# Kernel tuning notes

Measured on AMD Instinct MI355X. Metric: run time of the kernel, lower is better.

The kernel has to match this reference:

```python
import jax, jax.numpy as jnp
import numpy as np
import math

GRID_SIZE = 5
ORDER = 3
TAU = 0.1            # HuxleyRD tau (constructor default)
Q_SCALE = 64 / 2.0   # SaturatedQuantizer levels=64


def make_grid():
    h = 2.0 / GRID_SIZE
    # knots: arange(-order, grid_size+order+1)*h - 1  -> 12 values, shared by all in_features
    return jnp.arange(-ORDER, GRID_SIZE + ORDER + 1, dtype=jnp.float32) * h - 1.0


def b_splines(x, grid):
    # x: [b, in] -> bases: [b, in, GRID_SIZE+ORDER] via vectorized Cox-de Boor
    xg = x[..., None]
    g = grid  # [12], identical per feature so plain broadcasting suffices
    bases = ((xg >= g[:-1]) & (xg < g[1:])).astype(x.dtype)  # [b, in, 11]
    for p in range(1, ORDER + 1):
        t_i, t_ip = g[:-1 - p], g[p:-1]
        term1 = (xg - t_i) / (t_ip - t_i + 1e-8) * bases[..., :-1]
        t_i1, t_ip1 = g[1:-p], g[p + 1:]
        term2 = (t_ip1 - xg) / (t_ip1 - t_i1 + 1e-8) * bases[..., 1:]
        bases = term1 + term2
    return bases  # [b, in, 8]


def kan_layer(x, base_w, spline_w, grid):
    base = x @ base_w.T
    basis = b_splines(x, grid)
    # SaturatedQuantizer forward (round to levels); STE expressed via stop_gradient
    qw = spline_w + jax.lax.stop_gradient(jnp.round(spline_w * Q_SCALE) / Q_SCALE - spline_w)
    return base + jnp.einsum('bic,oic->bo', basis, qw)


def trig_unfolding(u, gcve_pressure, chirality, tau_decay):
    # u: [b, n]
    tr_c = jnp.sum(u * u, axis=-1)                                   # [b]
    uf_abs = jnp.abs(jnp.fft.rfft(u, axis=-1))                       # [b, n//2+1]
    det_pas = jnp.var(uf_abs, axis=-1, ddof=1) + 1e-6                # torch.var is unbiased
    denom = 2.0 * jnp.sqrt(det_pas) ** 3 + 1e-8
    cos_3phi = jnp.clip((3.0 * gcve_pressure - tr_c / tau_decay) / denom, -0.999, 0.999)
    phi = jnp.arccos(cos_3phi) / 3.0                                 # [b]
    lam_min = jnp.min(uf_abs, axis=-1)                               # [b]
    amp = 2.0 * jnp.sqrt(lam_min / 3.0 + 1e-8)                       # [b]
    ks = jnp.arange(3, dtype=u.dtype)                                # branch indices 0,1,2
    cos_terms = jnp.cos(phi[None, :] + 2.0 * jnp.pi * ks[:, None] / 3.0)   # [3, b]
    shifts = jnp.exp(-jnp.abs(chirality)[None, :] * ks[:, None])           # [3, b]
    coef = amp[None, :] * cos_terms * shifts                                # [3, b]
    branches = coef[:, :, None] * u[None, :, :]                             # [3, b, n]
    energies = jnp.linalg.norm(branches, axis=-1)                           # [3, b]
    best_k = jnp.argmax(energies, axis=0)                                   # [b]
    mask = (best_k[None, :] == jnp.arange(3)[:, None]).astype(u.dtype)      # [3, b]
    return jnp.sum(branches * mask[:, :, None], axis=0)


def huxley_rd(u, spectral_gate, kernel, a, gamma, tau_decay, soliton_velocity,
              gcve_pressure, chirality):
    N = u.shape[-1]
    # HarmonicWaveDecomposition: spectral sigmoid gate split
    uf = jnp.fft.rfft(u, axis=-1)
    gate = jax.nn.sigmoid(spectral_gate)
    u_erg = jnp.fft.irfft(uf * gate, n=N, axis=-1)
    u_ne = jnp.fft.irfft(uf * (1.0 - gate), n=N, axis=-1)
    # ergodic: cubic reaction + 3-tap diffusion conv (padding=1, cross-correlation)
    reaction = u_erg * (u_erg - a) * (1.0 - u_erg)
    up = jnp.pad(u_erg, ((0, 0), (1, 1)))
    diffusion = kernel[0] * up[:, :-2] + kernel[1] * up[:, 1:-1] + kernel[2] * up[:, 2:]
    u_erg_next = u_erg + TAU * (reaction + gamma * diffusion)
    # non-ergodic: spectral phase shift (soliton translation)
    nef = jnp.fft.rfft(u_ne, axis=-1)
    k_idx = jnp.arange(nef.shape[-1], dtype=jnp.float32)
    phase = jnp.exp(-1j * 2.0 * jnp.pi * k_idx * soliton_velocity / N)
    u_ne_shift = jnp.fft.irfft(nef * phase, n=N, axis=-1)
    u_ne_unf = trig_unfolding(u_ne_shift, gcve_pressure, chirality, tau_decay)
    s = u_erg_next + u_ne_unf
    return jax.nn.sigmoid(s) * s  # SiLU-style fusion


def setup_inputs() -> dict:
    key = jax.random.key(0)
    ks = jax.random.split(key, 12)
    B, NIN, W, NOUT = 4096, 512, 1024, 1024
    return {
        'c': jax.random.uniform(ks[0], (B, NIN), jnp.float32, -1.0, 1.0),
        'base_w0': jax.random.normal(ks[1], (W, NIN), jnp.float32) * (1.0 / np.sqrt(NIN)),
        'spline_w0': jax.random.normal(ks[2], (W, NIN, 8), jnp.float32) * 0.1,
        'base_w1': jax.random.normal(ks[3], (W, W), jnp.float32) * (1.0 / np.sqrt(W)),
        'spline_w1': jax.random.normal(ks[4], (W, W, 8), jnp.float32) * 0.1,
        'base_w2': jax.random.normal(ks[5], (NOUT, W), jnp.float32) * (1.0 / np.sqrt(W)),
        'spline_w2': jax.random.normal(ks[6], (NOUT, W, 8), jnp.float32) * 0.1,
        'spectral_gate': jnp.ones((NOUT // 2 + 1,), jnp.float32),
        'diffusion_kernel': jnp.asarray([0.1, -0.2, 0.1], jnp.float32),
        'a_param': jnp.asarray(0.1, jnp.float32),
        'gamma': jnp.asarray(1.0, jnp.float32),
        'tau_decay': jnp.asarray(0.1, jnp.float32),
        'soliton_velocity': jnp.asarray(0.25, jnp.float32),
        'gcve_pressure': jax.random.uniform(ks[7], (B,), jnp.float32),
        'chirality': jax.random.normal(ks[8], (B,), jnp.float32),
    }


def reference(c, base_w0, spline_w0, base_w1, spline_w1, base_w2, spline_w2,
              spectral_gate, diffusion_kernel, a_param, gamma, tau_decay,
              soliton_velocity, gcve_pressure, chirality):
    grid = make_grid()
    x = kan_layer(c, base_w0, spline_w0, grid)
    x = kan_layer(x, base_w1, spline_w1, grid)
    x = kan_layer(x, base_w2, spline_w2, grid)
    return huxley_rd(x, spectral_gate, diffusion_kernel, a_param, gamma,
                     tau_decay, soliton_velocity, gcve_pressure, chirality)
```

## Files before the change

### kernel.cpp

```cpp
#include <hip/hip_runtime.h>
#include <math.h>

typedef _Float16 f16;
typedef _Float16 f16x8 __attribute__((ext_vector_type(8)));
typedef float f32x4 __attribute__((ext_vector_type(4)));

__global__ __launch_bounds__(256) void expand_sum_a(
    const float* __restrict__ src, size_t plane, int Sin,
    f16* __restrict__ Aexp, int KIN, int shift)
{
    int idx = blockIdx.x * 256 + threadIdx.x;
    int i = idx & (KIN - 1);
    int b = idx >> shift;
    float x = 0.0f;
    for (int s = 0; s < Sin; ++s) x += src[(size_t)s * plane + idx];

    float xs = (x + 2.2f) * 2.5f;
    float fj = floorf(xs);
    int jj = (int)fj;
    float t = xs - fj;
    float t2 = t * t, t3 = t2 * t;
    float omt = 1.0f - t;
    float p0 = omt * omt * omt * (1.0f / 6.0f);
    float p1 = (3.0f * t3 - 6.0f * t2 + 4.0f) * (1.0f / 6.0f);
    float p2 = (-3.0f * t3 + 3.0f * t2 + 3.0f * t + 1.0f) * (1.0f / 6.0f);
    float p3 = t3 * (1.0f / 6.0f);

    union { f16 h[8]; uint4 v; } hi, lo;
    bool inr = (jj >= 0 && jj <= 10);
    #pragma unroll
    for (int cc = 0; cc < 8; ++cc) {
        int d = cc - (jj - 3);
        float v = 0.0f;
        if (inr) {
            if (d == 0) v = p0; else if (d == 1) v = p1;
            else if (d == 2) v = p2; else if (d == 3) v = p3;
        }
        f16 h = (f16)v;
        hi.h[cc] = h;
        lo.h[cc] = (f16)(v - (float)h);
    }
    size_t KEXP = (size_t)KIN * 19;
    f16* row = Aexp + (size_t)b * KEXP;
    *(uint4*)(row + (size_t)i * 8) = hi.v;
    *(uint4*)(row + (size_t)KIN * 8 + (size_t)i * 8) = lo.v;
    f16 xh = (f16)x;
    f16 xl = (f16)(x - (float)xh);
    int K16 = KIN * 16;
    row[K16 + i] = xh;
    row[K16 + KIN + i] = xh;
    row[K16 + 2 * KIN + i] = xl;
}

__global__ __launch_bounds__(256) void prep_b(
    const float* __restrict__ BW, const float* __restrict__ SW,
    f16* __restrict__ Bexp, int KIN, int shift)
{
    int idx = blockIdx.x * 256 + threadIdx.x;
    int i = idx & (KIN - 1);
    int o = idx >> shift;
    const float* sp = SW + ((size_t)o * KIN + i) * 8;
    union { f16 h[8]; uint4 v; } pk;
    #pragma unroll
    for (int cc = 0; cc < 8; ++cc)
        pk.h[cc] = (f16)(rintf(sp[cc] * 32.0f) * 0.03125f);
    size_t KEXP = (size_t)KIN * 19;
    f16* row = Bexp + (size_t)o * KEXP;
    *(uint4*)(row + (size_t)i * 8) = pk.v;
    *(uint4*)(row + (size_t)KIN * 8 + (size_t)i * 8) = pk.v;
    float w = BW[(size_t)o * KIN + i];
    f16 wh = (f16)w;
    f16 wl = (f16)(w - (float)wh);
    int K16 = KIN * 16;
    row[K16 + i] = wh;
    row[K16 + KIN + i] = wl;
    row[K16 + 2 * KIN + i] = wh;
}

__global__ __launch_bounds__(512, 2) void gemm_mfma(
    const f16* __restrict__ A, const f16* __restrict__ Bm,
    float* __restrict__ C, int Kfull, int Kc, size_t plane, int N)
{
    __shared__ __align__(16) f16 As[4][8192];
    __shared__ __align__(16) f16 Bs[4][8192];

    const int tid = threadIdx.x;
    const int wave = tid >> 6, lane = tid & 63;

    const int nwg = gridDim.x * gridDim.y * gridDim.z;
    const int b = blockIdx.x + gridDim.x * (blockIdx.y + gridDim.y * blockIdx.z);
    const int q = nwg >> 3;
    const int L = (b & 7) * q + (b >> 3);
    const int lx = L % gridDim.x;
    const int rest = L / gridDim.x;
    const int ly = rest % gridDim.y;
    const int lz = rest / gridDim.y;

    const int m0 = ly * 256, n0 = lx * 256;
    const int kb = lz * Kc;
    int kcl = Kfull - kb; if (kcl > Kc) kcl = Kc;
    const int NT = kcl >> 5;

    const int kc_src = (lane & 3) ^ ((lane >> 3) & 3);
    const f16* gb[4];
    int isA_[4], coff[4];
    #pragma unroll
    for (int j = 0; j < 4; ++j) {
        int cch = wave * 4 + j;
        int a = (cch < 16);
        int c8 = a ? cch : (cch - 16);
        int row0 = (a ? m0 : n0) + c8 * 16 + (lane >> 2);
        gb[j] = (a ? A : Bm) + (size_t)row0 * Kfull + kb + kc_src * 8;
        isA_[j] = a;
        coff[j] = c8 * 512;
    }

    f32x4 acc[8][4];
    #pragma unroll
    for (int i = 0; i < 8; ++i)
        #pragma unroll
        for (int j = 0; j < 4; ++j)
            acc[i][j] = (f32x4){0.f, 0.f, 0.f, 0.f};

    #pragma unroll
    for (int s = 0; s < 3; ++s) {
        if (s < NT) {
            int k0 = s << 5;
            #pragma unroll
            for (int j = 0; j < 4; ++j) {
                f16* dp = isA_[j] ? &As[s][coff[j]] : &Bs[s][coff[j]];
                __builtin_amdgcn_global_load_lds(
                    (const __attribute__((address_space(1))) unsigned int*)(gb[j] + k0),
                    (__attribute__((address_space(3))) unsigned int*)dp, 16, 0, 0);
            }
        }
    }
    if (NT >= 3)      asm volatile("s_waitcnt vmcnt(8)" ::: "memory");
    else if (NT == 2) asm volatile("s_waitcnt vmcnt(4)" ::: "memory");
    else              asm volatile("s_waitcnt vmcnt(0)" ::: "memory");
    __builtin_amdgcn_s_barrier();
    asm volatile("" ::: "memory");

    const int lr = lane & 15;
    const int ko = (((lane >> 4) ^ ((lr >> 1) & 3)) & 3) * 8;
    const int wm = (wave & 1) * 128, wn = (wave >> 1) * 64;

    for (int t = 0; t < NT; ++t) {
        const int st = t & 3;
        const int ns = (t + 3) & 3;
        const bool pf = (t + 3 < NT);
        const int kn = (t + 3) << 5;
        const int rem = NT - 1 - t;

        f16x8 af[4], bf[4], ag[4];
        #pragma unroll
        for (int i = 0; i < 4; ++i)
            af[i] = *(const f16x8*)&As[st][(wm + i * 16 + lr) * 32 + ko];
        #pragma unroll
        for (int j = 0; j < 4; ++j)
            bf[j] = *(const f16x8*)&Bs[st][(wn + j * 16 + lr) * 32 + ko];
        if (pf) {
            #pragma unroll
            for (int j = 0; j < 2; ++j) {
                f16* dp = isA_[j] ? &As[ns][coff[j]] : &Bs[ns][coff[j]];
                __builtin_amdgcn_global_load_lds(
                    (const __attribute__((address_space(1))) unsigned int*)(gb[j] + kn),
                    (__attribute__((address_space(3))) unsigned int*)dp, 16, 0, 0);
            }
        }
        #pragma unroll
        for (int i = 0; i < 4; ++i)
            ag[i] = *(const f16x8*)&As[st][(wm + 64 + i * 16 + lr) * 32 + ko];
        if (pf) {
            #pragma unroll
            for (int j = 2; j < 4; ++j) {
                f16* dp = isA_[j] ? &As[ns][coff[j]] : &Bs[ns][coff[j]];
                __builtin_amdgcn_global_load_lds(
                    (const __attribute__((address_space(1))) unsigned int*)(gb[j] + kn),
                    (__attribute__((address_space(3))) unsigned int*)dp, 16, 0, 0);
            }
        }

        asm volatile("s_waitcnt lgkmcnt(4)" ::: "memory");
        __builtin_amdgcn_sched_barrier(0);
        __builtin_amdgcn_s_setprio(1);
        #pragma unroll
        for (int i = 0; i < 4; ++i)
            #pragma unroll
            for (int j = 0; j < 4; ++j)
                acc[i][j] = __builtin_amdgcn_mfma_f32_16x16x32_f16(af[i], bf[j], acc[i][j], 0, 0, 0);
        __builtin_amdgcn_s_setprio(0);

        asm volatile("s_waitcnt lgkmcnt(0)" ::: "memory");
        __builtin_amdgcn_sched_barrier(0);
        __builtin_amdgcn_s_setprio(1);
        #pragma unroll
        for (int i = 0; i < 4; ++i)
            #pragma unroll
            for (int j = 0; j < 4; ++j)
                acc[4 + i][j] = __builtin_amdgcn_mfma_f32_16x16x32_f16(ag[i], bf[j], acc[4 + i][j], 0, 0, 0);
        __builtin_amdgcn_s_setprio(0);

        if (rem >= 3)      asm volatile("s_waitcnt vmcnt(8)" ::: "memory");
        else if (rem == 2) asm volatile("s_waitcnt vmcnt(4)" ::: "memory");
        else if (rem == 1) asm volatile("s_waitcnt vmcnt(0)" ::: "memory");
        if (rem >= 1) {
            __builtin_amdgcn_sched_barrier(0);
            __builtin_amdgcn_s_barrier();
            asm volatile("" ::: "memory");
        }
    }

    float* Cp = C + (size_t)lz * plane;
    #pragma unroll
    for (int i = 0; i < 8; ++i) {
        int row = m0 + wm + i * 16 + (lane >> 4) * 4;
        #pragma unroll
        for (int j = 0; j < 4; ++j) {
            int col = n0 + wn + j * 16 + lr;
            #pragma unroll
            for (int rr = 0; rr < 4; ++rr)
                Cp[(size_t)(row + rr) * N + col] = acc[i][j][rr];
        }
    }
}

__global__ __launch_bounds__(256) void kan_gemm(
    const float* __restrict__ X, const float* __restrict__ BW,
    const float* __restrict__ SW, float* __restrict__ Y, int KIN, int OUT)
{
    __shared__ __align__(16) float Asf[72][68];
    __shared__ __align__(16) float Bsf[72][68];
    const int tid = threadIdx.x;
    const int n0 = blockIdx.x * 64;
    const int m0 = blockIdx.y * 64;
    const int tx = tid & 15;
    const int ty = tid >> 4;
    float acc[4][4] = {};
    for (int k0 = 0; k0 < KIN; k0 += 8) {
        #pragma unroll
        for (int rep = 0; rep < 2; ++rep) {
            int idx = rep * 256 + tid;
            int r = idx >> 3, c = idx & 7;
            float x = X[(size_t)(m0 + r) * KIN + k0 + c];
            int bk = c * 9;
            Asf[bk][r] = x;
            #pragma unroll
            for (int z = 0; z < 8; ++z) Asf[bk + 1 + z][r] = 0.0f;
            float xs = (x + 2.2f) * 2.5f;
            float fj = floorf(xs);
            int j = (int)fj;
            if (j >= 0 && j <= 10) {
                float t = xs - fj;
                float t2 = t * t, t3 = t2 * t;
                float omt = 1.0f - t;
                float p0 = omt * omt * omt * (1.0f / 6.0f);
                float p1 = (3.0f * t3 - 6.0f * t2 + 4.0f) * (1.0f / 6.0f);
                float p2 = (-3.0f * t3 + 3.0f * t2 + 3.0f * t + 1.0f) * (1.0f / 6.0f);
                float p3 = t3 * (1.0f / 6.0f);
                if (j >= 3) Asf[bk + 1 + j - 3][r] = p0;
                if (j >= 2 && j <= 9) Asf[bk + 1 + j - 2][r] = p1;
                if (j >= 1 && j <= 8) Asf[bk + 1 + j - 1][r] = p2;
                if (j <= 7) Asf[bk + 1 + j][r] = p3;
            }
        }
        #pragma unroll
        for (int rep = 0; rep < 16; ++rep) {
            int idx = rep * 256 + tid;
            int ol = idx >> 6;
            int l = idx & 63;
            int i = l >> 3, cc = l & 7;
            float v = SW[((size_t)(n0 + ol) * KIN + k0 + i) * 8 + cc];
            Bsf[i * 9 + 1 + cc][ol] = rintf(v * 32.0f) * 0.03125f;
        }
        #pragma unroll
        for (int rep = 0; rep < 2; ++rep) {
            int idx = rep * 256 + tid;
            int ol = idx >> 3, cc = idx & 7;
            Bsf[cc * 9][ol] = BW[(size_t)(n0 + ol) * KIN + k0 + cc];
        }
        __syncthreads();
        #pragma unroll 8
        for (int kk = 0; kk < 72; ++kk) {
            float4 av = *(const float4*)&Asf[kk][ty * 4];
            float4 bv = *(const float4*)&Bsf[kk][tx * 4];
            acc[0][0] += av.x * bv.x; acc[0][1] += av.x * bv.y; acc[0][2] += av.x * bv.z; acc[0][3] += av.x * bv.w;
            acc[1][0] += av.y * bv.x; acc[1][1] += av.y * bv.y; acc[1][2] += av.y * bv.z; acc[1][3] += av.y * bv.w;
            acc[2][0] += av.z * bv.x; acc[2][1] += av.z * bv.y; acc[2][2] += av.z * bv.z; acc[2][3] += av.z * bv.w;
            acc[3][0] += av.w * bv.x; acc[3][1] += av.w * bv.y; acc[3][2] += av.w * bv.z; acc[3][3] += av.w * bv.w;
        }
        __syncthreads();
    }
    #pragma unroll
    for (int i = 0; i < 4; ++i) {
        float4 o = make_float4(acc[i][0], acc[i][1], acc[i][2], acc[i][3]);
        *(float4*)&Y[(size_t)(m0 + ty * 4 + i) * OUT + n0 + tx * 4] = o;
    }
}

__device__ __forceinline__ float block_reduce_sum(float v, float* red, int tid) {
    red[tid] = v; __syncthreads();
    #pragma unroll
    for (int s = 128; s > 0; s >>= 1) {
        if (tid < s) red[tid] += red[tid + s];
        __syncthreads();
    }
    float r = red[0]; __syncthreads();
    return r;
}
__device__ __forceinline__ float block_reduce_min(float v, float* red, int tid) {
    red[tid] = v; __syncthreads();
    #pragma unroll
    for (int s = 128; s > 0; s >>= 1) {
        if (tid < s) red[tid] = fminf(red[tid], red[tid + s]);
        __syncthreads();
    }
    float r = red[0]; __syncthreads();
    return r;
}

__device__ void fft1024(float2* X, const float2* tw, int tid, bool inverse) {
    if (!inverse) {
        for (int sh = 9; sh >= 0; --sh) {
            int h = 1 << sh;
            #pragma unroll
            for (int q = 0; q < 2; ++q) {
                int b = tid + q * 256;
                int g = b >> sh, j = b & (h - 1);
                int i0 = (g << (sh + 1)) + j, i1 = i0 + h;
                float2 u = X[i0], v = X[i1];
                float dx = u.x - v.x, dy = u.y - v.y;
                X[i0] = make_float2(u.x + v.x, u.y + v.y);
                float2 w = tw[j << (9 - sh)];
                X[i1] = make_float2(dx * w.x + dy * w.y, dy * w.x - dx * w.y);
            }
            __syncthreads();
        }
    } else {
        for (int sh = 0; sh <= 9; ++sh) {
            int h = 1 << sh;
            #pragma unroll
            for (int q = 0; q < 2; ++q) {
                int b = tid + q * 256;
                int g = b >> sh, j = b & (h - 1);
                int i0 = (g << (sh + 1)) + j, i1 = i0 + h;
                float2 u = X[i0], v = X[i1];
                float2 w = tw[j << (9 - sh)];
                float tx2 = v.x * w.x - v.y * w.y;
                float ty2 = v.x * w.y + v.y * w.x;
                X[i0] = make_float2(u.x + tx2, u.y + ty2);
                X[i1] = make_float2(u.x - tx2, u.y - ty2);
            }
            __syncthreads();
        }
    }
}

__global__ __launch_bounds__(256) void huxley_kernel(
    const float* __restrict__ Pin, size_t plane, int S,
    float* __restrict__ dst,
    const float* __restrict__ sg, const float* __restrict__ dk,
    const float* __restrict__ pa, const float* __restrict__ pgam,
    const float* __restrict__ ptau, const float* __restrict__ pvel,
    const float* __restrict__ gp, const float* __restrict__ chi)
{
    __shared__ float2 A[1024];
    __shared__ float2 Bb[1024];
    __shared__ float sErg[1024];
    __shared__ float sAbs[516];
    __shared__ float2 tw[512];
    __shared__ float red[256];
    __shared__ float sG[516];

    const int tid = threadIdx.x;
    const int row = blockIdx.x;
    const float* pin = Pin + (size_t)row * 1024;
    float* uo = dst + (size_t)row * 1024;

    for (int m = tid; m < 512; m += 256) {
        float s, c;
        sincosf(6.283185307179586f * (float)m * (1.0f / 1024.0f), &s, &c);
        tw[m] = make_float2(c, s);
    }
    for (int k = tid; k < 513; k += 256)
        sG[k] = 1.0f / (1.0f + expf(-sg[k]));
    for (int i = tid; i < 1024; i += 256) {
        float s = 0.0f;
        for (int ss = 0; ss < S; ++ss) s += pin[(size_t)ss * plane + i];
        A[i] = make_float2(s, 0.0f);
    }
    __syncthreads();

    fft1024(A, tw, tid, false);

    for (int p = tid; p < 1024; p += 256) {
        int k = (int)(__brev((unsigned)p) >> 22);
        int m = (k <= 512) ? k : 1024 - k;
        float g = sG[m] * (1.0f / 1024.0f);
        Bb[p] = make_float2(A[p].x * g, A[p].y * g);
    }
    __syncthreads();
    fft1024(Bb, tw, tid, true);
    for (int i = tid; i < 1024; i += 256) sErg[i] = Bb[i].x;
    __syncthreads();

    const float vv = pvel[0];
    for (int p = tid; p < 1024; p += 256) {
        int k = (int)(__brev((unsigned)p) >> 22);
        int m = (k <= 512) ? k : 1024 - k;
        float omg = 1.0f - sG[m];
        float nx = A[p].x * omg, ny = A[p].y * omg;
        float ang = (k <= 512)
            ? (-6.283185307179586f * vv * (float)k * (1.0f / 1024.0f))
            : (6.283185307179586f * vv * (float)(1024 - k) * (1.0f / 1024.0f));
        float sn, cs;
        sincosf(ang, &sn, &cs);
        float yx = nx * cs - ny * sn;
        float yy = nx * sn + ny * cs;
        if (k < 512)       sAbs[k]   = sqrtf(nx * nx + ny * ny);
        else if (k == 512) sAbs[512] = fabsf(yx);
        Bb[p] = make_float2(yx * (1.0f / 1024.0f), yy * (1.0f / 1024.0f));
    }
    __syncthreads();
    fft1024(Bb, tw, tid, true);

    float loc = 0.0f;
    for (int i = tid; i < 1024; i += 256) { float x = Bb[i].x; loc += x * x; }
    float trc = block_reduce_sum(loc, red, tid);

    loc = 0.0f;
    for (int k = tid; k < 513; k += 256) loc += sAbs[k];
    float mean = block_reduce_sum(loc, red, tid) * (1.0f / 513.0f);

    loc = 0.0f;
    for (int k = tid; k < 513; k += 256) { float d = sAbs[k] - mean; loc += d * d; }
    float varsum = block_reduce_sum(loc, red, tid);

    loc = 3.4e38f;
    for (int k = tid; k < 513; k += 256) loc = fminf(loc, sAbs[k]);
    float lmin = block_reduce_min(loc, red, tid);

    float det_pas = varsum * (1.0f / 512.0f) + 1e-6f;
    float sd = sqrtf(det_pas);
    float denom = 2.0f * sd * sd * sd + 1e-8f;
    float c3 = (3.0f * gp[row] - trc / ptau[0]) / denom;
    c3 = fminf(fmaxf(c3, -0.999f), 0.999f);
    float ph = acosf(c3) * (1.0f / 3.0f);
    float amp = 2.0f * sqrtf(lmin * (1.0f / 3.0f) + 1e-8f);
    float nu = sqrtf(trc);
    float achi = fabsf(chi[row]);
    float cbest = 0.0f, ebest = -1.0f;
    #pragma unroll
    for (int kb = 0; kb < 3; ++kb) {
        float ck = amp * cosf(ph + 2.0943951023931953f * (float)kb) * expf(-achi * (float)kb);
        float ek = fabsf(ck) * nu;
        if (ek > ebest) { ebest = ek; cbest = ck; }
    }

    const float a = pa[0], gm = pgam[0];
    const float k0 = dk[0], k1 = dk[1], k2 = dk[2];
    for (int i = tid; i < 1024; i += 256) {
        float e = sErg[i];
        float l = (i > 0) ? sErg[i - 1] : 0.0f;
        float r = (i < 1023) ? sErg[i + 1] : 0.0f;
        float reac = e * (e - a) * (1.0f - e);
        float diff = k0 * l + k1 * e + k2 * r;
        float un = e + 0.1f * (reac + gm * diff);
        float s = un + cbest * Bb[i].x;
        uo[i] = s / (1.0f + expf(-s));
    }
}


extern "C" void kernel_launch(void* const* d_in, const int* in_sizes, int n_in,
                              void* d_out, int out_size, void* d_ws, size_t ws_size,
                              hipStream_t stream) {
    const float* c    = (const float*)d_in[0];
    const float* bw0  = (const float*)d_in[1];
    const float* sw0  = (const float*)d_in[2];
    const float* bw1  = (const float*)d_in[3];
    const float* sw1  = (const float*)d_in[4];
    const float* bw2  = (const float*)d_in[5];
    const float* sw2  = (const float*)d_in[6];
    const float* sg   = (const float*)d_in[7];
    const float* dk   = (const float*)d_in[8];
    const float* pa   = (const float*)d_in[9];
    const float* pgam = (const float*)d_in[10];
    const float* ptau = (const float*)d_in[11];
    const float* pvel = (const float*)d_in[12];
    const float* gp   = (const float*)d_in[13];
    const float* chi  = (const float*)d_in[14];

    const int B = 4096, NIN = 512, W = 1024, NOUT = 1024;
    const int KE0 = 19 * NIN, KE1 = 19 * W;
    const size_t MN = (size_t)B * W;
    const size_t BE = (size_t)W * KE1 * 2;
    dim3 blk(256);
    dim3 gblk(512);

    struct Cand { int CH, S; };
    const Cand cands[] = {
        {4096, 4}, {4096, 3}, {2048, 4}, {2048, 3}, {1024, 4},
        {512, 4}, {256, 4}
    };
    int CH = 0, S = 1;
    for (const auto& cd : cands) {
        size_t need = BE + (size_t)cd.CH * KE1 * 2 + (size_t)cd.S * MN * 4;
        if (need <= ws_size) { CH = cd.CH; S = cd.S; break; }
    }

    if (CH > 0) {
        f16* Bexp = (f16*)d_ws;
        float* P  = (float*)((char*)d_ws + BE);
        f16* Aexp = (f16*)((char*)d_ws + BE + (size_t)S * MN * 4);

        const int Kc0 = ((KE0 / 32 + S - 1) / S) * 32;
        const int Kc1 = ((KE1 / 32 + S - 1) / S) * 32;

        prep_b<<<(W * NIN) / 256, blk, 0, stream>>>(bw0, sw0, Bexp, NIN, 9);
        for (int r0 = 0; r0 < B; r0 += CH) {
            expand_sum_a<<<(CH * NIN) / 256, blk, 0, stream>>>(
                c + (size_t)r0 * NIN, 0, 1, Aexp, NIN, 9);
            gemm_mfma<<<dim3(W / 256, CH / 256, S), gblk, 0, stream>>>(
                Aexp, Bexp, P + (size_t)r0 * W, KE0, Kc0, MN, W);
        }
        prep_b<<<(W * W) / 256, blk, 0, stream>>>(bw1, sw1, Bexp, W, 10);
        for (int r0 = 0; r0 < B; r0 += CH) {
            expand_sum_a<<<(CH * W) / 256, blk, 0, stream>>>(
                P + (size_t)r0 * W, MN, S, Aexp, W, 10);
            gemm_mfma<<<dim3(W / 256, CH / 256, S), gblk, 0, stream>>>(
                Aexp, Bexp, P + (size_t)r0 * W, KE1, Kc1, MN, W);
        }
        prep_b<<<(NOUT * W) / 256, blk, 0, stream>>>(bw2, sw2, Bexp, W, 10);
        for (int r0 = 0; r0 < B; r0 += CH) {
            expand_sum_a<<<(CH * W) / 256, blk, 0, stream>>>(
                P + (size_t)r0 * W, MN, S, Aexp, W, 10);
            gemm_mfma<<<dim3(NOUT / 256, CH / 256, S), gblk, 0, stream>>>(
                Aexp, Bexp, P + (size_t)r0 * W, KE1, Kc1, MN, NOUT);
        }
        huxley_kernel<<<B, blk, 0, stream>>>(P, MN, S, (float*)d_out,
                                             sg, dk, pa, pgam, ptau, pvel, gp, chi);
    } else {
        float* fx0 = (float*)d_ws;
        float* fx1 = fx0 + (size_t)B * W;
        dim3 g0(W / 64, B / 64);
        kan_gemm<<<g0, blk, 0, stream>>>(c,   bw0, sw0, fx0, NIN, W);
        kan_gemm<<<g0, blk, 0, stream>>>(fx0, bw1, sw1, fx1, W,   W);
        dim3 g2(NOUT / 64, B / 64);
        kan_gemm<<<g2, blk, 0, stream>>>(fx1, bw2, sw2, (float*)d_out, W, NOUT);
        huxley_kernel<<<B, blk, 0, stream>>>((float*)d_out, 0, 1, (float*)d_out,
                                             sg, dk, pa, pgam, ptau, pvel, gp, chi);
    }
}
```

Measured before the change: 678.2 us.

## Pack two real rows into one complex FFT in huxley kernel

The huxley kernel now handles two batch rows per block by placing them in the real and imaginary parts of a single complex 1024-point FFT. Each row's spectral magnitudes are recovered through conjugate-symmetric separation, and the reductions and elementwise epilogue run on float2 pairs. This halves the FFT work and the block count per row, at the price of more shared memory per block and a dependence on B being even.

New measurement: 670.5 us. Within noise of the previous version (-1.1%).

```diff
diff --git a/kernel.cpp b/kernel.cpp
--- a/kernel.cpp
+++ b/kernel.cpp
@@ -298,24 +298,30 @@
     }
 }
 
-__device__ __forceinline__ float block_reduce_sum(float v, float* red, int tid) {
+__device__ __forceinline__ float2 block_reduce_sum2(float2 v, float2* red, int tid) {
     red[tid] = v; __syncthreads();
     #pragma unroll
     for (int s = 128; s > 0; s >>= 1) {
-        if (tid < s) red[tid] += red[tid + s];
+        if (tid < s) {
+            red[tid].x += red[tid + s].x;
+            red[tid].y += red[tid + s].y;
+        }
         __syncthreads();
     }
-    float r = red[0]; __syncthreads();
+    float2 r = red[0]; __syncthreads();
     return r;
 }
-__device__ __forceinline__ float block_reduce_min(float v, float* red, int tid) {
+__device__ __forceinline__ float2 block_reduce_min2(float2 v, float2* red, int tid) {
     red[tid] = v; __syncthreads();
     #pragma unroll
     for (int s = 128; s > 0; s >>= 1) {
-        if (tid < s) red[tid] = fminf(red[tid], red[tid + s]);
+        if (tid < s) {
+            red[tid].x = fminf(red[tid].x, red[tid + s].x);
+            red[tid].y = fminf(red[tid].y, red[tid + s].y);
+        }
         __syncthreads();
     }
-    float r = red[0]; __syncthreads();
+    float2 r = red[0]; __syncthreads();
     return r;
 }
 
@@ -366,16 +372,19 @@
 {
     __shared__ float2 A[1024];
     __shared__ float2 Bb[1024];
-    __shared__ float sErg[1024];
-    __shared__ float sAbs[516];
+    __shared__ float2 sErg[1024];
+    __shared__ float sAbs1[516];
+    __shared__ float sAbs2[516];
     __shared__ float2 tw[512];
-    __shared__ float red[256];
+    __shared__ float2 red2[256];
     __shared__ float sG[516];
 
     const int tid = threadIdx.x;
-    const int row = blockIdx.x;
-    const float* pin = Pin + (size_t)row * 1024;
-    float* uo = dst + (size_t)row * 1024;
+    const int r0 = blockIdx.x * 2;
+    const float* pin0 = Pin + (size_t)r0 * 1024;
+    const float* pin1 = Pin + (size_t)(r0 + 1) * 1024;
+    float* uo0 = dst + (size_t)r0 * 1024;
+    float* uo1 = dst + (size_t)(r0 + 1) * 1024;
 
     for (int m = tid; m < 512; m += 256) {
         float s, c;
@@ -385,9 +394,12 @@
     for (int k = tid; k < 513; k += 256)
         sG[k] = 1.0f / (1.0f + expf(-sg[k]));
     for (int i = tid; i < 1024; i += 256) {
-        float s = 0.0f;
-        for (int ss = 0; ss < S; ++ss) s += pin[(size_t)ss * plane + i];
-        A[i] = make_float2(s, 0.0f);
+        float s0 = 0.0f, s1 = 0.0f;
+        for (int ss = 0; ss < S; ++ss) {
+            s0 += pin0[(size_t)ss * plane + i];
+            s1 += pin1[(size_t)ss * plane + i];
+        }
+        A[i] = make_float2(s0, s1);
     }
     __syncthreads();
 
@@ -401,7 +413,7 @@
     }
     __syncthreads();
     fft1024(Bb, tw, tid, true);
-    for (int i = tid; i < 1024; i += 256) sErg[i] = Bb[i].x;
+    for (int i = tid; i < 1024; i += 256) sErg[i] = Bb[i];
     __syncthreads();
 
     const float vv = pvel[0];
@@ -409,65 +421,107 @@
         int k = (int)(__brev((unsigned)p) >> 22);
         int m = (k <= 512) ? k : 1024 - k;
         float omg = 1.0f - sG[m];
-        float nx = A[p].x * omg, ny = A[p].y * omg;
+        float2 z = A[p];
+        float nx = z.x * omg, ny = z.y * omg;
         float ang = (k <= 512)
             ? (-6.283185307179586f * vv * (float)k * (1.0f / 1024.0f))
             : (6.283185307179586f * vv * (float)(1024 - k) * (1.0f / 1024.0f));
         float sn, cs;
         sincosf(ang, &sn, &cs);
-        float yx = nx * cs - ny * sn;
-        float yy = nx * sn + ny * cs;
-        if (k < 512)       sAbs[k]   = sqrtf(nx * nx + ny * ny);
-        else if (k == 512) sAbs[512] = fabsf(yx);
+        float yx, yy;
+        if (k == 512) {
+            yx = nx * cs;
+            yy = ny * cs;
+            sAbs1[512] = fabsf(nx * cs);
+            sAbs2[512] = fabsf(ny * cs);
+        } else {
+            yx = nx * cs - ny * sn;
+            yy = nx * sn + ny * cs;
+            if (k < 512) {
+                int p2 = (int)(__brev((unsigned)((1024 - k) & 1023)) >> 22);
+                float2 z2 = A[p2];
+                float f1x = 0.5f * (z.x + z2.x), f1y = 0.5f * (z.y - z2.y);
+                float f2x = 0.5f * (z.y + z2.y), f2y = 0.5f * (z2.x - z.x);
+                sAbs1[k] = omg * sqrtf(f1x * f1x + f1y * f1y);
+                sAbs2[k] = omg * sqrtf(f2x * f2x + f2y * f2y);
+            }
+        }
         Bb[p] = make_float2(yx * (1.0f / 1024.0f), yy * (1.0f / 1024.0f));
     }
     __syncthreads();
     fft1024(Bb, tw, tid, true);
 
-    float loc = 0.0f;
-    for (int i = tid; i < 1024; i += 256) { float x = Bb[i].x; loc += x * x; }
-    float trc = block_reduce_sum(loc, red, tid);
-
-    loc = 0.0f;
-    for (int k = tid; k < 513; k += 256) loc += sAbs[k];
-    float mean = block_reduce_sum(loc, red, tid) * (1.0f / 513.0f);
-
-    loc = 0.0f;
-    for (int k = tid; k < 513; k += 256) { float d = sAbs[k] - mean; loc += d * d; }
-    float varsum = block_reduce_sum(loc, red, tid);
-
-    loc = 3.4e38f;
-    for (int k = tid; k < 513; k += 256) loc = fminf(loc, sAbs[k]);
-    float lmin = block_reduce_min(loc, red, tid);
-
-    float det_pas = varsum * (1.0f / 512.0f) + 1e-6f;
-    float sd = sqrtf(det_pas);
-    float denom = 2.0f * sd * sd * sd + 1e-8f;
-    float c3 = (3.0f * gp[row] - trc / ptau[0]) / denom;
-    c3 = fminf(fmaxf(c3, -0.999f), 0.999f);
-    float ph = acosf(c3) * (1.0f / 3.0f);
-    float amp = 2.0f * sqrtf(lmin * (1.0f / 3.0f) + 1e-8f);
-    float nu = sqrtf(trc);
-    float achi = fabsf(chi[row]);
-    float cbest = 0.0f, ebest = -1.0f;
-    #pragma unroll
-    for (int kb = 0; kb < 3; ++kb) {
-        float ck = amp * cosf(ph + 2.0943951023931953f * (float)kb) * expf(-achi * (float)kb);
-        float ek = fabsf(ck) * nu;
-        if (ek > ebest) { ebest = ek; cbest = ck; }
+    float2 loc = make_float2(0.0f, 0.0f);
+    for (int i = tid; i < 1024; i += 256) {
+        loc.x += Bb[i].x * Bb[i].x;
+        loc.y += Bb[i].y * Bb[i].y;
+    }
+    float2 trc = block_reduce_sum2(loc, red2, tid);
+
+    loc = make_float2(0.0f, 0.0f);
+    for (int k = tid; k < 513; k += 256) { loc.x += sAbs1[k]; loc.y += sAbs2[k]; }
+    float2 msum = block_reduce_sum2(loc, red2, tid);
+    float2 mean = make_float2(msum.x * (1.0f / 513.0f), msum.y * (1.0f / 513.0f));
+
+    loc = make_float2(0.0f, 0.0f);
+    for (int k = tid; k < 513; k += 256) {
+        float d1 = sAbs1[k] - mean.x;
+        float d2 = sAbs2[k] - mean.y;
+        loc.x += d1 * d1; loc.y += d2 * d2;
+    }
+    float2 varsum = block_reduce_sum2(loc, red2, tid);
+
+    loc = make_float2(3.4e38f, 3.4e38f);
+    for (int k = tid; k < 513; k += 256) {
+        loc.x = fminf(loc.x, sAbs1[k]);
+        loc.y = fminf(loc.y, sAbs2[k]);
+    }
+    float2 lmin = block_reduce_min2(loc, red2, tid);
+
+    const float tauv = ptau[0];
+    float trcv[2]  = { trc.x, trc.y };
+    float varv[2]  = { varsum.x, varsum.y };
+    float lminv[2] = { lmin.x, lmin.y };
+    float gpv[2]   = { gp[r0], gp[r0 + 1] };
+    float chv[2]   = { chi[r0], chi[r0 + 1] };
+    float cb[2];
+    #pragma unroll
+    for (int rr = 0; rr < 2; ++rr) {
+        float det_pas = varv[rr] * (1.0f / 512.0f) + 1e-6f;
+        float sd = sqrtf(det_pas);
+        float denom = 2.0f * sd * sd * sd + 1e-8f;
+        float c3 = (3.0f * gpv[rr] - trcv[rr] / tauv) / denom;
+        c3 = fminf(fmaxf(c3, -0.999f), 0.999f);
+        float ph = acosf(c3) * (1.0f / 3.0f);
+        float amp = 2.0f * sqrtf(lminv[rr] * (1.0f / 3.0f) + 1e-8f);
+        float nu = sqrtf(trcv[rr]);
+        float achi = fabsf(chv[rr]);
+        float cbest = 0.0f, ebest = -1.0f;
+        #pragma unroll
+        for (int kb = 0; kb < 3; ++kb) {
+            float ck = amp * cosf(ph + 2.0943951023931953f * (float)kb) * expf(-achi * (float)kb);
+            float ek = fabsf(ck) * nu;
+            if (ek > ebest) { ebest = ek; cbest = ck; }
+        }
+        cb[rr] = cbest;
     }
 
     const float a = pa[0], gm = pgam[0];
     const float k0 = dk[0], k1 = dk[1], k2 = dk[2];
     for (int i = tid; i < 1024; i += 256) {
-        float e = sErg[i];
-        float l = (i > 0) ? sErg[i - 1] : 0.0f;
-        float r = (i < 1023) ? sErg[i + 1] : 0.0f;
-        float reac = e * (e - a) * (1.0f - e);
-        float diff = k0 * l + k1 * e + k2 * r;
-        float un = e + 0.1f * (reac + gm * diff);
-        float s = un + cbest * Bb[i].x;
-        uo[i] = s / (1.0f + expf(-s));
+        float2 e = sErg[i];
+        float2 l = (i > 0) ? sErg[i - 1] : make_float2(0.0f, 0.0f);
+        float2 r = (i < 1023) ? sErg[i + 1] : make_float2(0.0f, 0.0f);
+        float reac1 = e.x * (e.x - a) * (1.0f - e.x);
+        float diff1 = k0 * l.x + k1 * e.x + k2 * r.x;
+        float un1 = e.x + 0.1f * (reac1 + gm * diff1);
+        float s1 = un1 + cb[0] * Bb[i].x;
+        uo0[i] = s1 / (1.0f + expf(-s1));
+        float reac2 = e.y * (e.y - a) * (1.0f - e.y);
+        float diff2 = k0 * l.y + k1 * e.y + k2 * r.y;
+        float un2 = e.y + 0.1f * (reac2 + gm * diff2);
+        float s2 = un2 + cb[1] * Bb[i].y;
+        uo1[i] = s2 / (1.0f + expf(-s2));
     }
 }
 
@@ -538,8 +592,8 @@
             gemm_mfma<<<dim3(NOUT / 256, CH / 256, S), gblk, 0, stream>>>(
                 Aexp, Bexp, P + (size_t)r0 * W, KE1, Kc1, MN, NOUT);
         }
-        huxley_kernel<<<B, blk, 0, stream>>>(P, MN, S, (float*)d_out,
-                                             sg, dk, pa, pgam, ptau, pvel, gp, chi);
+        huxley_kernel<<<B / 2, blk, 0, stream>>>(P, MN, S, (float*)d_out,
+                                                 sg, dk, pa, pgam, ptau, pvel, gp, chi);
     } else {
         float* fx0 = (float*)d_ws;
         float* fx1 = fx0 + (size_t)B * W;
@@ -548,7 +602,7 @@
         kan_gemm<<<g0, blk, 0, stream>>>(fx0, bw1, sw1, fx1, W,   W);
         dim3 g2(NOUT / 64, B / 64);
         kan_gemm<<<g2, blk, 0, stream>>>(fx1, bw2, sw2, (float*)d_out, W, NOUT);
-        huxley_kernel<<<B, blk, 0, stream>>>((float*)d_out, 0, 1, (float*)d_out,
-                                             sg, dk, pa, pgam, ptau, pvel, gp, chi);
-    }
-}
+        huxley_kernel<<<B / 2, blk, 0, stream>>>((float*)d_out, 0, 1, (float*)d_out,
+                                                 sg, dk, pa, pgam, ptau, pvel, gp, chi);
+    }
+}
```
